# Optimization experiments

Hardware: AMD Instinct MI355X
Metric: run time of the kernel (lower is better)

## Reference

```python
import jax, jax.numpy as jnp
import numpy as np

H_IMG, W_IMG = 32, 32   # img_dim
HID = 256               # hidden_size
B = 128                 # batch


def setup_inputs() -> dict:
    key = jax.random.key(0)
    k1, k2, k3, k4 = jax.random.split(key, 4)
    x = jax.random.normal(k1, (B, H_IMG * W_IMG), dtype=jnp.float32)
    w_ih = jax.random.normal(k2, (4 * HID, 1), dtype=jnp.float32) * 0.1
    w_hh = jax.random.normal(k3, (4 * HID, HID), dtype=jnp.float32) * 0.05
    bias = jax.random.normal(k4, (4 * HID,), dtype=jnp.float32) * 0.1
    return {"x": x, "w_ih": w_ih, "w_hh": w_hh, "bias": bias}


def _mdlstm(x, w_ih, w_hh, bias):
    # x: [B, H*W] in row-major pixel order (pixel_idx = row*W + col)
    Bb = x.shape[0]
    xg = x.reshape(Bb, H_IMG, W_IMG).transpose(1, 2, 0)  # [H, W, B]
    wih_vec = w_ih[:, 0]  # input_size == 1 -> linear is scalar * row-vector

    def cell(x_pix, h_up, s_up, h_left, s_left):
        # Same weight_hh is applied to both directional hidden states; for
        # boundary pixels the corresponding h/s are zeros, so the gating in
        # the original code (skip when row==0 / col==0) holds identically.
        gates = (x_pix[:, None] * wih_vec[None, :]
                 + (h_up + h_left) @ w_hh.T
                 + bias)                                  # [B, 4*HID]
        i, f, g, o = jnp.split(gates, 4, axis=1)
        i = jax.nn.sigmoid(i)
        f = jax.nn.sigmoid(f)
        g = jnp.tanh(g)
        o = jax.nn.sigmoid(o)
        s = f * (s_up + s_left) + i * g                   # shared forgetgate for both dims
        h = o * jnp.tanh(s)
        return h, s

    zeros = jnp.zeros((Bb, HID), x.dtype)

    def row_step(carry, x_row):
        h_up_row, s_up_row = carry                        # [W, B, HID] each

        def col_step(c, inp):
            h_left, s_left = c
            x_pix, h_up, s_up = inp
            h, s = cell(x_pix, h_up, s_up, h_left, s_left)
            return (h, s), (h, s)

        _, (h_row, s_row) = jax.lax.scan(col_step, (zeros, zeros),
                                         (x_row, h_up_row, s_up_row))
        return (h_row, s_row), h_row

    init = (jnp.zeros((W_IMG, Bb, HID), x.dtype),
            jnp.zeros((W_IMG, Bb, HID), x.dtype))
    _, h_all = jax.lax.scan(row_step, init, xg)           # [H, W, B, HID]
    # torch.cat(h_matrix, 1): pixels ordered row-major, each [B, HID]
    return h_all.transpose(2, 0, 1, 3).reshape(Bb, H_IMG * W_IMG * HID)


def reference(x, w_ih, w_hh, bias):
    return _mdlstm(x, w_ih, w_hh, bias)
```

## Files before the change

### kernel.cpp

```cpp
#include <hip/hip_runtime.h>
#include <math.h>


#define HIMG 32
#define WIMG 32
#define BATCH 128
#define HID 256
#define BH (BATCH * HID)
#define SLAB (32 * 128 * 256)

#define WSTRIDE 516

__global__ __launch_bounds__(256, 4)
void mdlstm_diag_kernel(const float* __restrict__ x,
                        const float* __restrict__ wih,
                        const float* __restrict__ whh,
                        const float* __restrict__ bias,
                        float* __restrict__ out,
                        double* __restrict__ hbuf,
                        double* __restrict__ sbuf,
                        int d, int rlo)
{
    __shared__ double A_lds[1024];
    __shared__ float  W_lds[8 * WSTRIDE];

    const int tid = threadIdx.x;
    const int id  = blockIdx.x;
    const int cellIdx = id >> 5;
    const int tileIdx = id & 31;
    const int ktile = tileIdx & 7;
    const int b4    = tileIdx >> 3;
    const int k0 = ktile * 32;
    const int b0 = b4 * 32;

    const int r = rlo + cellIdx;
    const int c = d - r;
    const int rc = r * WIMG + c;

    const int prev = (d & 1) ^ 1;
    const int cur  = d & 1;
    const double* hp = hbuf + (size_t)prev * SLAB;
    const double* sp = sbuf + (size_t)prev * SLAB;
    double* hc = hbuf + (size_t)cur * SLAB;
    double* sc = sbuf + (size_t)cur * SLAB;

    const bool has_up   = (r > 0);
    const bool has_left = (c > 0);
    const double* hu = hp + (size_t)(r - 1) * BH;
    const double* hl = hp + (size_t)r * BH;

    const int tx = tid & 31;
    const int ty = tid >> 5;

    const int a_bl = tid >> 4;
    const int a_k  = (tid & 15) * 2;
    const size_t ga0 = (size_t)(b0 + a_bl) * HID + a_k;
    const size_t ga1 = ga0 + (size_t)16 * HID;
    const float* w_src[4];
    #pragma unroll
    for (int p = 0; p < 4; p++) {
        int f = tid + p * 256;
        int row = f >> 3;
        int g = row >> 5, j = row & 31;
        w_src[p] = whh + (size_t)(g * 256 + k0 + j) * HID + (f & 7) * 4;
    }

    double acc[4][4];
    #pragma unroll
    for (int g = 0; g < 4; g++)
        #pragma unroll
        for (int i = 0; i < 4; i++) acc[g][i] = 0.0;

    double2 pu0, pl0, pu1, pl1;
    float4 pw[4];
    {
        const double2 z = {0.0, 0.0};
        pu0 = has_up   ? *(const double2*)(hu + ga0) : z;
        pu1 = has_up   ? *(const double2*)(hu + ga1) : z;
        pl0 = has_left ? *(const double2*)(hl + ga0) : z;
        pl1 = has_left ? *(const double2*)(hl + ga1) : z;
        #pragma unroll
        for (int p = 0; p < 4; p++)
            pw[p] = *(const float4*)(w_src[p]);
    }

    for (int ck = 0; ck < 8; ck++) {
        __syncthreads();
        double2 s0, s1;
        s0.x = pu0.x + pl0.x; s0.y = pu0.y + pl0.y;
        s1.x = pu1.x + pl1.x; s1.y = pu1.y + pl1.y;
        *(double2*)&A_lds[2 * tid] = s0;
        *(double2*)&A_lds[512 + 2 * tid] = s1;
        #pragma unroll
        for (int p = 0; p < 4; p++) {
            int f = tid + p * 256;
            *(float4*)&W_lds[(f & 7) * WSTRIDE + (f >> 3) * 4] = pw[p];
        }
        __syncthreads();

        if (ck < 7) {
            const int kk = (ck + 1) * 32;
            const double2 z = {0.0, 0.0};
            pu0 = has_up   ? *(const double2*)(hu + ga0 + kk) : z;
            pu1 = has_up   ? *(const double2*)(hu + ga1 + kk) : z;
            pl0 = has_left ? *(const double2*)(hl + ga0 + kk) : z;
            pl1 = has_left ? *(const double2*)(hl + ga1 + kk) : z;
            #pragma unroll
            for (int p = 0; p < 4; p++)
                pw[p] = *(const float4*)(w_src[p] + kk);
        }

        #pragma unroll
        for (int tg = 0; tg < 8; tg++) {
            double2 ad[4][2];
            #pragma unroll
            for (int i = 0; i < 4; i++) {
                const int bl = ty + 8 * i;
                ad[i][0] = *(const double2*)&A_lds[bl * 32 + tg * 4];
                ad[i][1] = *(const double2*)&A_lds[bl * 32 + tg * 4 + 2];
            }
            #pragma unroll
            for (int g = 0; g < 4; g++) {
                const float4 wf = *(const float4*)&W_lds[tg * WSTRIDE + (g * 32 + tx) * 4];
                const double w0 = (double)wf.x, w1 = (double)wf.y;
                const double w2 = (double)wf.z, w3 = (double)wf.w;
                #pragma unroll
                for (int i = 0; i < 4; i++) {
                    double t = acc[g][i];
                    t = fma(ad[i][0].x, w0, t);
                    t = fma(ad[i][0].y, w1, t);
                    t = fma(ad[i][1].x, w2, t);
                    t = fma(ad[i][1].y, w3, t);
                    acc[g][i] = t;
                }
            }
        }
    }

    const int k = k0 + tx;
    double wv[4], bv[4];
    #pragma unroll
    for (int g = 0; g < 4; g++) {
        wv[g] = (double)wih[g * 256 + k];
        bv[g] = (double)bias[g * 256 + k];
    }
    #pragma unroll
    for (int i = 0; i < 4; i++) {
        const int b = b0 + ty + 8 * i;
        const double xp = (double)x[b * (HIMG * WIMG) + rc];
        const double su = has_up   ? sp[(size_t)(r - 1) * BH + b * HID + k] : 0.0;
        const double sl = has_left ? sp[(size_t)r * BH + b * HID + k]       : 0.0;
        const double gi = acc[0][i] + xp * wv[0] + bv[0];
        const double gf = acc[1][i] + xp * wv[1] + bv[1];
        const double gg = acc[2][i] + xp * wv[2] + bv[2];
        const double go = acc[3][i] + xp * wv[3] + bv[3];
        const double iv = 1.0 / (1.0 + exp(-gi));
        const double fv = 1.0 / (1.0 + exp(-gf));
        const double gv = tanh(gg);
        const double ov = 1.0 / (1.0 + exp(-go));
        const double sv = fv * (su + sl) + iv * gv;
        const double hv = ov * tanh(sv);
        sc[(size_t)r * BH + b * HID + k] = sv;
        hc[(size_t)r * BH + b * HID + k] = hv;
        out[(size_t)b * (HIMG * WIMG * HID) + (size_t)rc * HID + k] = (float)hv;
    }
}

extern "C" void kernel_launch(void* const* d_in, const int* in_sizes, int n_in,
                              void* d_out, int out_size, void* d_ws, size_t ws_size,
                              hipStream_t stream) {
    const float* x    = (const float*)d_in[0];
    const float* wih  = (const float*)d_in[1];
    const float* whh  = (const float*)d_in[2];
    const float* bias = (const float*)d_in[3];
    float* out = (float*)d_out;

    double* hbuf = (double*)d_ws;
    double* sbuf = hbuf + (size_t)2 * SLAB;

    for (int d = 0; d < HIMG + WIMG - 1; d++) {
        int rlo = d - (WIMG - 1); if (rlo < 0) rlo = 0;
        int rhi = d < (HIMG - 1) ? d : (HIMG - 1);
        int nc = rhi - rlo + 1;
        mdlstm_diag_kernel<<<dim3(nc * 32), 256, 0, stream>>>(
            x, wih, whh, bias, out, hbuf, sbuf, d, rlo);
    }
}
```

Before: 3.570 ms.

## Use FP64 MFMA for recurrent gate matmul with runtime layout detection

Replaces the scalar double FMA inner product with the 16x16x4 FP64 MFMA instruction, transposing A and W tiles in LDS into k-major swizzled layouts. A runtime probe MFMA detects the accumulator lane layout, and a scalar fallback path is kept. Results are then scattered through LDS to restore the per-thread layout for the gate epilogue. This adds an extra LDS round trip, scalar LDS stores and a probe per block, in exchange for matrix-core throughput.

```diff
diff --git a/kernel.cpp b/kernel.cpp
--- a/kernel.cpp
+++ b/kernel.cpp
@@ -9,7 +9,9 @@
 #define BH (BATCH * HID)
 #define SLAB (32 * 128 * 256)
 
-#define WSTRIDE 516
+#define WSTRIDE 136
+
+typedef double f64x4 __attribute__((ext_vector_type(4)));
 
 __global__ __launch_bounds__(256, 4)
 void mdlstm_diag_kernel(const float* __restrict__ x,
@@ -21,8 +23,10 @@
                         double* __restrict__ sbuf,
                         int d, int rlo)
 {
-    __shared__ double A_lds[1024];
-    __shared__ float  W_lds[8 * WSTRIDE];
+    __shared__ double lds[4096];
+    double* A_lds = lds;
+    float*  W_lds = (float*)(lds + 1024);
+    double* G_lds = lds;
 
     const int tid = threadIdx.x;
     const int id  = blockIdx.x;
@@ -49,29 +53,56 @@
     const double* hu = hp + (size_t)(r - 1) * BH;
     const double* hl = hp + (size_t)r * BH;
 
-    const int tx = tid & 31;
-    const int ty = tid >> 5;
-
-    const int a_bl = tid >> 4;
-    const int a_k  = (tid & 15) * 2;
-    const size_t ga0 = (size_t)(b0 + a_bl) * HID + a_k;
+    const int lane = tid & 63;
+    const int wid  = tid >> 6;
+    const int wb0  = (wid & 1) * 16;
+    const int wf0  = (wid >> 1) * 64;
+    const int cc   = lane & 15;
+    const int gg   = lane >> 4;
+
+    int layout;
+    {
+        double pa = (cc == 1) ? 1.0 : 0.0;
+        double pb = (cc == 2) ? 1.0 : 0.0;
+        f64x4 pc = {0.0, 0.0, 0.0, 0.0};
+        pc = __builtin_amdgcn_mfma_f64_16x16x4f64(pa, pb, pc, 0, 0, 0);
+        double s = fabs(pc[0]) + fabs(pc[1]) + fabs(pc[2]) + fabs(pc[3]);
+        #pragma unroll
+        for (int off = 32; off > 0; off >>= 1) s += __shfl_xor(s, off, 64);
+        unsigned long long h0 = __ballot(lane == 2  && pc[1] == 4.0);
+        unsigned long long h1 = __ballot(lane == 18 && pc[0] == 4.0);
+        unsigned long long h2 = __ballot(lane == 1  && pc[2] == 4.0);
+        unsigned long long h3 = __ballot(lane == 33 && pc[0] == 4.0);
+        layout = -1;
+        if (s == 4.0) {
+            if (h0) layout = 0;
+            else if (h1) layout = 1;
+            else if (h2) layout = 2;
+            else if (h3) layout = 3;
+        }
+    }
+    const bool use_mfma = (layout >= 0);
+
+    const int a_row = tid >> 4;
+    const int a_kp  = tid & 15;
+    const size_t ga0 = (size_t)(b0 + a_row) * HID + 2 * a_kp;
     const size_t ga1 = ga0 + (size_t)16 * HID;
     const float* w_src[4];
+    int w_phi[4], w_kq[4];
     #pragma unroll
     for (int p = 0; p < 4; p++) {
-        int f = tid + p * 256;
-        int row = f >> 3;
-        int g = row >> 5, j = row & 31;
-        w_src[p] = whh + (size_t)(g * 256 + k0 + j) * HID + (f & 7) * 4;
-    }
-
-    double acc[4][4];
-    #pragma unroll
-    for (int g = 0; g < 4; g++)
-        #pragma unroll
-        for (int i = 0; i < 4; i++) acc[g][i] = 0.0;
-
-    double2 pu0, pl0, pu1, pl1;
+        int u = tid + p * 256;
+        int phi = u >> 3, kq = u & 7;
+        int F = (phi >> 5) * 256 + k0 + (phi & 31);
+        w_src[p] = whh + (size_t)F * HID + 4 * kq;
+        w_phi[p] = phi; w_kq[p] = kq;
+    }
+
+    f64x4 acc[4];
+    #pragma unroll
+    for (int ft = 0; ft < 4; ft++) acc[ft] = (f64x4){0.0, 0.0, 0.0, 0.0};
+
+    double2 pu0, pu1, pl0, pl1;
     float4 pw[4];
     {
         const double2 z = {0.0, 0.0};
@@ -86,58 +117,86 @@
 
     for (int ck = 0; ck < 8; ck++) {
         __syncthreads();
-        double2 s0, s1;
-        s0.x = pu0.x + pl0.x; s0.y = pu0.y + pl0.y;
-        s1.x = pu1.x + pl1.x; s1.y = pu1.y + pl1.y;
-        *(double2*)&A_lds[2 * tid] = s0;
-        *(double2*)&A_lds[512 + 2 * tid] = s1;
+        {
+            const int k = 2 * a_kp;
+            const double s0x = pu0.x + pl0.x, s0y = pu0.y + pl0.y;
+            const double s1x = pu1.x + pl1.x, s1y = pu1.y + pl1.y;
+            A_lds[ k      * 32 + ((a_row      + k    ) & 31)] = s0x;
+            A_lds[(k + 1) * 32 + ((a_row      + k + 1) & 31)] = s0y;
+            A_lds[ k      * 32 + ((a_row + 16 + k    ) & 31)] = s1x;
+            A_lds[(k + 1) * 32 + ((a_row + 16 + k + 1) & 31)] = s1y;
+        }
         #pragma unroll
         for (int p = 0; p < 4; p++) {
-            int f = tid + p * 256;
-            *(float4*)&W_lds[(f & 7) * WSTRIDE + (f >> 3) * 4] = pw[p];
+            const int kb = 4 * w_kq[p];
+            W_lds[(kb + 0) * WSTRIDE + w_phi[p]] = pw[p].x;
+            W_lds[(kb + 1) * WSTRIDE + w_phi[p]] = pw[p].y;
+            W_lds[(kb + 2) * WSTRIDE + w_phi[p]] = pw[p].z;
+            W_lds[(kb + 3) * WSTRIDE + w_phi[p]] = pw[p].w;
         }
         __syncthreads();
 
         if (ck < 7) {
-            const int kk = (ck + 1) * 32;
+            const int kg = (ck + 1) * 32;
             const double2 z = {0.0, 0.0};
-            pu0 = has_up   ? *(const double2*)(hu + ga0 + kk) : z;
-            pu1 = has_up   ? *(const double2*)(hu + ga1 + kk) : z;
-            pl0 = has_left ? *(const double2*)(hl + ga0 + kk) : z;
-            pl1 = has_left ? *(const double2*)(hl + ga1 + kk) : z;
+            pu0 = has_up   ? *(const double2*)(hu + ga0 + kg) : z;
+            pu1 = has_up   ? *(const double2*)(hu + ga1 + kg) : z;
+            pl0 = has_left ? *(const double2*)(hl + ga0 + kg) : z;
+            pl1 = has_left ? *(const double2*)(hl + ga1 + kg) : z;
             #pragma unroll
             for (int p = 0; p < 4; p++)
-                pw[p] = *(const float4*)(w_src[p] + kk);
-        }
-
-        #pragma unroll
-        for (int tg = 0; tg < 8; tg++) {
-            double2 ad[4][2];
+                pw[p] = *(const float4*)(w_src[p] + kg);
+        }
+
+        if (use_mfma) {
             #pragma unroll
-            for (int i = 0; i < 4; i++) {
-                const int bl = ty + 8 * i;
-                ad[i][0] = *(const double2*)&A_lds[bl * 32 + tg * 4];
-                ad[i][1] = *(const double2*)&A_lds[bl * 32 + tg * 4 + 2];
-            }
-            #pragma unroll
-            for (int g = 0; g < 4; g++) {
-                const float4 wf = *(const float4*)&W_lds[tg * WSTRIDE + (g * 32 + tx) * 4];
-                const double w0 = (double)wf.x, w1 = (double)wf.y;
-                const double w2 = (double)wf.z, w3 = (double)wf.w;
-                #pragma unroll
-                for (int i = 0; i < 4; i++) {
-                    double t = acc[g][i];
-                    t = fma(ad[i][0].x, w0, t);
-                    t = fma(ad[i][0].y, w1, t);
-                    t = fma(ad[i][1].x, w2, t);
-                    t = fma(ad[i][1].y, w3, t);
-                    acc[g][i] = t;
+            for (int t = 0; t < 8; t++) {
+                const int kq = t * 4 + gg;
+                const double aval = A_lds[kq * 32 + ((wb0 + cc + kq) & 31)];
+                const float* wrow = &W_lds[kq * WSTRIDE + wf0 + cc];
+                #pragma unroll
+                for (int ft = 0; ft < 4; ft++) {
+                    const double bval = (double)wrow[ft * 16];
+                    acc[ft] = __builtin_amdgcn_mfma_f64_16x16x4f64(aval, bval, acc[ft], 0, 0, 0);
                 }
             }
-        }
-    }
-
-    const int k = k0 + tx;
+        } else {
+            for (int k = 0; k < 32; k++) {
+                double av[4], wv4[4];
+                #pragma unroll
+                for (int b = 0; b < 4; b++)
+                    av[b] = A_lds[k * 32 + ((wb0 + 4 * gg + b + k) & 31)];
+                #pragma unroll
+                for (int ft = 0; ft < 4; ft++)
+                    wv4[ft] = (double)W_lds[k * WSTRIDE + wf0 + ft * 16 + cc];
+                #pragma unroll
+                for (int ft = 0; ft < 4; ft++)
+                    #pragma unroll
+                    for (int b = 0; b < 4; b++)
+                        acc[ft][b] = fma(av[b], wv4[ft], acc[ft][b]);
+            }
+        }
+    }
+
+    __syncthreads();
+    const int slay = use_mfma ? layout : 0;
+    #pragma unroll
+    for (int ft = 0; ft < 4; ft++) {
+        #pragma unroll
+        for (int b = 0; b < 4; b++) {
+            const int rA = (slay & 1) ? (gg + 4 * b) : (4 * gg + b);
+            const int m  = (slay >= 2) ? cc : rA;
+            const int n  = (slay >= 2) ? rA : cc;
+            const int phi  = wf0 + ft * 16 + n;
+            const int brow = wb0 + m;
+            G_lds[phi * 32 + ((brow + phi) & 31)] = acc[ft][b];
+        }
+    }
+    __syncthreads();
+
+    const int ec = tid & 31;
+    const int eb = tid >> 5;
+    const int k = k0 + ec;
     double wv[4], bv[4];
     #pragma unroll
     for (int g = 0; g < 4; g++) {
@@ -146,17 +205,24 @@
     }
     #pragma unroll
     for (int i = 0; i < 4; i++) {
-        const int b = b0 + ty + 8 * i;
+        const int bl = eb + 8 * i;
+        const int b = b0 + bl;
+        double gate[4];
+        #pragma unroll
+        for (int g = 0; g < 4; g++) {
+            const int phi = g * 32 + ec;
+            gate[g] = G_lds[phi * 32 + ((bl + phi) & 31)];
+        }
         const double xp = (double)x[b * (HIMG * WIMG) + rc];
         const double su = has_up   ? sp[(size_t)(r - 1) * BH + b * HID + k] : 0.0;
         const double sl = has_left ? sp[(size_t)r * BH + b * HID + k]       : 0.0;
-        const double gi = acc[0][i] + xp * wv[0] + bv[0];
-        const double gf = acc[1][i] + xp * wv[1] + bv[1];
-        const double gg = acc[2][i] + xp * wv[2] + bv[2];
-        const double go = acc[3][i] + xp * wv[3] + bv[3];
+        const double gi = gate[0] + xp * wv[0] + bv[0];
+        const double gf = gate[1] + xp * wv[1] + bv[1];
+        const double gg2 = gate[2] + xp * wv[2] + bv[2];
+        const double go = gate[3] + xp * wv[3] + bv[3];
         const double iv = 1.0 / (1.0 + exp(-gi));
         const double fv = 1.0 / (1.0 + exp(-gf));
-        const double gv = tanh(gg);
+        const double gv = tanh(gg2);
         const double ov = 1.0 / (1.0 + exp(-go));
         const double sv = fv * (su + sl) + iv * gv;
         const double hv = ov * tanh(sv);
```

Result: faster. 3.143 ms (-11.9%).
